# Performance work log

Measured on AMD Instinct MI355X. Metric: run time of the kernel, lower is better.

Reference implementation:

```python
import jax, jax.numpy as jnp
from jax import lax
import numpy as np

B, C_IN, C_OUT, H, W, K = 4, 128, 256, 64, 64, 3
KK = K * K
MID = C_IN // 4
EPS = 1e-5


def conv2d(x, w, b, pad, groups=1):
    out = lax.conv_general_dilated(x, w, (1, 1), [(pad, pad), (pad, pad)],
                                   feature_group_count=groups,
                                   dimension_numbers=('NCHW', 'OIHW', 'NCHW'))
    return out + b[None, :, None, None]


def bnorm(x, g, b, m, v):
    # inference-mode BatchNorm2d
    scale = (g / jnp.sqrt(v + EPS))
    return (x - m[None, :, None, None]) * scale[None, :, None, None] + b[None, :, None, None]


def bilinear_gather(x, py, px):
    # x: (B,C,H,W); py/px: (B,KK,H,W) float sample coords; zero outside bounds
    Bb, C, Hh, Ww = x.shape
    xf = x.reshape(Bb, C, Hh * Ww)
    y0 = jnp.floor(py)
    x0 = jnp.floor(px)
    wy1 = py - y0
    wx1 = px - x0

    def corner(yc, xc, wgt):
        valid = (yc >= 0) & (yc <= Hh - 1) & (xc >= 0) & (xc <= Ww - 1)
        yi = jnp.clip(yc, 0, Hh - 1).astype(jnp.int32)
        xi = jnp.clip(xc, 0, Ww - 1).astype(jnp.int32)
        idx = (yi * Ww + xi).reshape(Bb, -1)  # (B, KK*H*W)
        g = jax.vmap(lambda f, i: f[:, i])(xf, idx).reshape(Bb, C, *py.shape[1:])
        return g * (wgt * valid)[:, None]

    return (corner(y0, x0, (1 - wy1) * (1 - wx1))
            + corner(y0, x0 + 1, (1 - wy1) * wx1)
            + corner(y0 + 1, x0, wy1 * (1 - wx1))
            + corner(y0 + 1, x0 + 1, wy1 * wx1))


def deform_conv2d(x, offset, mask, w, b, pad=1):
    # modulated deformable conv v2, stride=1, dilation=1, groups=1, dg=1
    Bb, C, Hh, Ww = x.shape
    off = offset.reshape(Bb, KK, 2, Hh, Ww)  # (dy,dx) per kernel point
    k = jnp.arange(KK)
    ky = (k // K).astype(x.dtype)
    kx = (k % K).astype(x.dtype)
    py = (jnp.arange(Hh, dtype=x.dtype) - pad)[None, None, :, None] + ky[None, :, None, None] + off[:, :, 0]
    px = (jnp.arange(Ww, dtype=x.dtype) - pad)[None, None, None, :] + kx[None, :, None, None] + off[:, :, 1]
    val = bilinear_gather(x, py, px) * mask[:, None]  # (B,C,KK,H,W)
    return jnp.einsum('bckhw,ock->bohw', val, w.reshape(w.shape[0], C, KK)) + b[None, :, None, None]


def setup_inputs() -> dict:
    key = jax.random.key(0)
    ks = iter(jax.random.split(key, 40))

    def P(shape, scale=0.05):
        return jax.random.normal(next(ks), shape, jnp.float32) * scale

    d = {}
    d['x'] = jax.random.normal(next(ks), (B, C_IN, H, W), jnp.float32)
    # DCConv offset branch
    d['oc1_w'] = P((MID, C_IN, 3, 3)); d['oc1_b'] = P((MID,))
    d['obn_g'] = jnp.ones((MID,)); d['obn_b'] = jnp.zeros((MID,))
    d['obn_m'] = jnp.zeros((MID,)); d['obn_v'] = jnp.ones((MID,))
    d['oc2_w'] = P((2 * KK, MID, 3, 3), 0.01); d['oc2_b'] = P((2 * KK,), 0.01)
    # DCConv mask branch
    d['mc1_w'] = P((MID, C_IN, 3, 3)); d['mc1_b'] = P((MID,))
    d['mbn_g'] = jnp.ones((MID,)); d['mbn_b'] = jnp.zeros((MID,))
    d['mbn_m'] = jnp.zeros((MID,)); d['mbn_v'] = jnp.ones((MID,))
    d['mc2_w'] = P((KK, MID, 3, 3), 0.01); d['mc2_b'] = jnp.ones((KK,))
    # DCConv main weight
    d['dc_w'] = P((C_OUT, C_IN, 3, 3)); d['dc_b'] = jnp.zeros((C_OUT,))
    # contour branch: depthwise 3x3 + BN + ReLU + 1x1
    d['cb_dw_w'] = P((C_IN, 1, 3, 3)); d['cb_dw_b'] = P((C_IN,))
    d['cbn_g'] = jnp.ones((C_IN,)); d['cbn_b'] = jnp.zeros((C_IN,))
    d['cbn_m'] = jnp.zeros((C_IN,)); d['cbn_v'] = jnp.ones((C_IN,))
    d['cb_pw_w'] = P((C_OUT // 2, C_IN, 1, 1)); d['cb_pw_b'] = P((C_OUT // 2,))
    # spatial attention 7x7 -> 1 channel
    d['sa_w'] = P((1, C_OUT + C_OUT // 2, 7, 7)); d['sa_b'] = jnp.zeros((1,))
    # fusion 1x1 + BN + ReLU
    d['fu_w'] = P((C_OUT, C_OUT + C_OUT // 2, 1, 1)); d['fu_b'] = jnp.zeros((C_OUT,))
    d['fbn_g'] = jnp.ones((C_OUT,)); d['fbn_b'] = jnp.zeros((C_OUT,))
    d['fbn_m'] = jnp.zeros((C_OUT,)); d['fbn_v'] = jnp.ones((C_OUT,))
    return d


def reference(x, oc1_w, oc1_b, obn_g, obn_b, obn_m, obn_v, oc2_w, oc2_b,
              mc1_w, mc1_b, mbn_g, mbn_b, mbn_m, mbn_v, mc2_w, mc2_b,
              dc_w, dc_b, cb_dw_w, cb_dw_b, cbn_g, cbn_b, cbn_m, cbn_v,
              cb_pw_w, cb_pw_b, sa_w, sa_b, fu_w, fu_b, fbn_g, fbn_b, fbn_m, fbn_v):
    # DCConv: offsets + sigmoid masks + modulated deformable conv
    h = jax.nn.relu(bnorm(conv2d(x, oc1_w, oc1_b, 1), obn_g, obn_b, obn_m, obn_v))
    offset = conv2d(h, oc2_w, oc2_b, 1)
    hm = jax.nn.relu(bnorm(conv2d(x, mc1_w, mc1_b, 1), mbn_g, mbn_b, mbn_m, mbn_v))
    mask = jax.nn.sigmoid(conv2d(hm, mc2_w, mc2_b, 1))
    main_feat = deform_conv2d(x, offset, mask, dc_w, dc_b, pad=1)
    # contour branch
    hc = jax.nn.relu(bnorm(conv2d(x, cb_dw_w, cb_dw_b, 1, groups=C_IN), cbn_g, cbn_b, cbn_m, cbn_v))
    contour_feat = conv2d(hc, cb_pw_w, cb_pw_b, 0)
    combined = jnp.concatenate([main_feat, contour_feat], axis=1)
    attn = jax.nn.sigmoid(conv2d(combined, sa_w, sa_b, 3))
    combined = combined * attn
    return jax.nn.relu(bnorm(conv2d(combined, fu_w, fu_b, 0), fbn_g, fbn_b, fbn_m, fbn_v))
```

## Files before the change

kernel.cpp:

```cpp
#include <hip/hip_runtime.h>
#include <hip/hip_bf16.h>
#include <math.h>

#define BN   4
#define CIN  128
#define COUT 256
#define HWP  4096

typedef __hip_bfloat16 bf16;
typedef __attribute__((ext_vector_type(8))) short sh8;
typedef __attribute__((ext_vector_type(4))) float f32x4;

__device__ __forceinline__ float b2f(bf16 v) { return __bfloat162float(v); }
__device__ __forceinline__ float bflo(unsigned u) { return __uint_as_float(u << 16); }
__device__ __forceinline__ float bfhi(unsigned u) { return __uint_as_float(u & 0xffff0000u); }
__device__ __forceinline__ unsigned short f2bfbits(float f) {
    union { bf16 h; unsigned short u; } cv; cv.h = __float2bfloat16(f); return cv.u;
}
__device__ __forceinline__ float bfj(const uint4& c, int j) {
    unsigned u = (&c.x)[j >> 1];
    return (j & 1) ? bfhi(u) : bflo(u);
}

__global__ __launch_bounds__(256) void transpose_x_kernel(const float* __restrict__ x,
                                                          bf16* __restrict__ xt)
{
    __shared__ bf16 t[64][136];
    const int b = blockIdx.x >> 6, chunk = blockIdx.x & 63;
    const int pos0 = chunk * 64;
    const int tid = threadIdx.x;
    const int lane = tid & 63, wv = tid >> 6;
    const float* xb = x + (size_t)b * CIN * HWP + pos0 + lane;
    #pragma unroll 4
    for (int j = 0; j < 32; j++) {
        int ci = wv * 32 + j;
        t[lane][ci] = __float2bfloat16(xb[(size_t)ci * HWP]);
    }
    __syncthreads();
    const int p = tid >> 2, cig = tid & 3;
    uint4* dst = (uint4*)(xt + ((size_t)b * HWP + pos0 + p) * 128 + cig * 32);
    const uint4* src = (const uint4*)&t[p][cig * 32];
    #pragma unroll
    for (int q = 0; q < 4; q++) dst[q] = src[q];
}

__global__ __launch_bounds__(256) void prep_all_kernel(
    const float* __restrict__ dc_w,
    const float* __restrict__ oc1_w, const float* __restrict__ oc1_b,
    const float* __restrict__ obn_g, const float* __restrict__ obn_b,
    const float* __restrict__ obn_m, const float* __restrict__ obn_v,
    const float* __restrict__ mc1_w, const float* __restrict__ mc1_b,
    const float* __restrict__ mbn_g, const float* __restrict__ mbn_b,
    const float* __restrict__ mbn_m, const float* __restrict__ mbn_v,
    const float* __restrict__ fu_w, const float* __restrict__ fu_b,
    const float* __restrict__ fbn_g, const float* __restrict__ fbn_b,
    const float* __restrict__ fbn_m, const float* __restrict__ fbn_v,
    const float* __restrict__ sa_w,
    const float* __restrict__ oc2_w, const float* __restrict__ mc2_w,
    const float* __restrict__ cb_pw_w,
    const float* __restrict__ cb_dw_b, const float* __restrict__ cbn_g,
    const float* __restrict__ cbn_b, const float* __restrict__ cbn_m,
    const float* __restrict__ cbn_v,
    bf16* __restrict__ wBf2, bf16* __restrict__ wCf, float* __restrict__ ab,
    bf16* __restrict__ wFf, bf16* __restrict__ wSAf, float* __restrict__ fab,
    bf16* __restrict__ wDf, bf16* __restrict__ wPf, float* __restrict__ dwab)
{
    int o = blockIdx.x * 256 + threadIdx.x;
    if (o < 294912) {
        int j = o & 7, o2 = o >> 3;
        int lane = o2 & 63, t = o2 >> 6;
        int l16 = lane & 15, quad = lane >> 4;
        int mt = t & 3, t2 = t >> 2;
        int kt = t2 % 18, t3 = t2 / 18;
        int h = t3 & 1, wv = t3 >> 1;
        int co = wv * 64 + mt * 16 + l16;
        int kkh = kt * 32 + quad * 8 + j;
        int k = kkh >> 6, ci = h * 64 + (kkh & 63);
        wBf2[o] = __float2bfloat16(dc_w[co * 1152 + ci * 9 + k]);
    } else if (o < 368640) {
        int idx = o - 294912;
        int j = idx & 7, o2 = idx >> 3;
        int lane = o2 & 63, t = o2 >> 6;
        int l16 = lane & 15, quad = lane >> 4;
        int kt = t % 36, wv = t / 36;
        int co = wv * 16 + l16;
        int kk = kt * 32 + quad * 8 + j;
        int k = kk >> 7, ci = kk & 127;
        float v = (co < 32) ? oc1_w[co * 1152 + ci * 9 + k]
                            : mc1_w[(co - 32) * 1152 + ci * 9 + k];
        wCf[idx] = __float2bfloat16(v);
    } else if (o < 368704) {
        int c = o - 368640;
        float g, bb, m, vv, bias;
        if (c < 32) { g = obn_g[c]; bb = obn_b[c]; m = obn_m[c]; vv = obn_v[c]; bias = oc1_b[c]; }
        else { int c2 = c - 32; g = mbn_g[c2]; bb = mbn_b[c2]; m = mbn_m[c2]; vv = mbn_v[c2]; bias = mc1_b[c2]; }
        float alpha = g / sqrtf(vv + 1e-5f);
        ab[c] = alpha;
        ab[64 + c] = (bias - m) * alpha + bb;
    } else if (o < 467008) {
        int idx = o - 368704;
        int j = idx & 7, o2 = idx >> 3;
        int lane = o2 & 63, t = o2 >> 6;
        int l16 = lane & 15, quad = lane >> 4;
        int mt = t & 3, t2 = t >> 2;
        int kt = t2 % 12, wv = t2 / 12;
        int co = wv * 64 + mt * 16 + l16;
        int kk = kt * 32 + quad * 8 + j;
        wFf[idx] = __float2bfloat16(fu_w[co * 384 + kk]);
    } else if (o < 491584) {
        int idx = o - 467008;
        int j = idx & 7, o2 = idx >> 3;
        int lane = o2 & 63, t = o2 >> 6;
        int l16 = lane & 15, quad = lane >> 4;
        int kt = t % 12, wv = t / 12;
        int jr = wv * 16 + l16;
        int kk = kt * 32 + quad * 8 + j;
        wSAf[idx] = (jr < 49) ? __float2bfloat16(sa_w[kk * 49 + jr]) : __float2bfloat16(0.f);
    } else if (o < 491840) {
        int co = o - 491584;
        float alpha = fbn_g[co] / sqrtf(fbn_v[co] + 1e-5f);
        fab[co] = alpha;
        fab[256 + co] = (fu_b[co] - fbn_m[co]) * alpha + fbn_b[co];
    } else if (o < 510272) {
        int idx = o - 491840;
        int j = idx & 7, o2 = idx >> 3;
        int lane = o2 & 63, t = o2 >> 6;
        int l16 = lane & 15, quad = lane >> 4;
        int mt = t & 1, kt = t >> 1;
        int co = mt * 16 + l16;
        int kk = kt * 32 + quad * 8 + j;
        int k = kk >> 6, c = kk & 63;
        float v = 0.f;
        if (co < 18 && c < 32) v = oc2_w[co * 288 + c * 9 + k];
        else if (co >= 18 && co < 27 && c >= 32) v = mc2_w[(co - 18) * 288 + (c - 32) * 9 + k];
        wDf[idx] = __float2bfloat16(v);
    } else if (o < 526656) {
        int idx = o - 510272;
        int j = idx & 7, o2 = idx >> 3;
        int lane = o2 & 63, t = o2 >> 6;
        int l16 = lane & 15, quad = lane >> 4;
        int wv = t >> 3, kt = (t >> 1) & 3, mt = t & 1;
        int co = wv * 32 + mt * 16 + l16;
        int kk = kt * 32 + quad * 8 + j;
        wPf[idx] = __float2bfloat16(cb_pw_w[co * 128 + kk]);
    } else if (o < 526784) {
        int c = o - 526656;
        float alpha = cbn_g[c] / sqrtf(cbn_v[c] + 1e-5f);
        dwab[c] = alpha;
        dwab[128 + c] = (cb_dw_b[c] - cbn_m[c]) * alpha + cbn_b[c];
    }
}

__global__ __launch_bounds__(256) void conv1_mfma_kernel(
    const bf16* __restrict__ xt, const bf16* __restrict__ wCf, const float* __restrict__ ab,
    bf16* __restrict__ ht)
{
    __shared__ __align__(16) bf16 val[16][1160];

    const int bid = blockIdx.x;
    const int b = (bid & 7) >> 1;
    const int tile = ((bid >> 3) << 1) | (bid & 1);
    const int pos0 = tile * 16;
    const int y = tile >> 2, x0 = (tile & 3) * 16;
    const int tid = threadIdx.x;
    const int cig = tid & 15, pix = tid >> 4;
    const int ci0 = cig * 8;
    const int xxp = x0 + pix;

    const bf16* xtb = xt + (size_t)b * HWP * 128;
    #pragma unroll
    for (int k = 0; k < 9; k++) {
        int yy = y + k / 3 - 1, xx = xxp + k % 3 - 1;
        bool valid = (yy >= 0 && yy <= 63 && xx >= 0 && xx <= 63);
        uint4 c = {0, 0, 0, 0};
        if (valid) c = *(const uint4*)(xtb + (size_t)(yy * 64 + xx) * 128 + ci0);
        *(uint4*)&val[pix][k * 128 + ci0] = c;
    }
    __syncthreads();

    const int lane = tid & 63, wv = tid >> 6;
    const int quad = lane >> 4, l16 = lane & 15;
    f32x4 acc = {0, 0, 0, 0};
    const bf16* wl0 = wCf + (size_t)wv * 36 * 512 + lane * 8;
    const bf16* vbase = &val[l16][quad * 8];

    sh8 af = *(const sh8*)(wl0);
    sh8 bf = *(const sh8*)(vbase);
    sh8 afn, bfn;
    for (int kt = 0; kt < 36; kt++) {
        if (kt < 35) {
            afn = *(const sh8*)(wl0 + (kt + 1) * 512);
            bfn = *(const sh8*)(vbase + (kt + 1) * 32);
        }
        acc = __builtin_amdgcn_mfma_f32_16x16x32_bf16(af, bf, acc, 0, 0, 0);
        af = afn; bf = bfn;
    }

    float o0 = fmaxf(acc[0] * ab[wv * 16 + quad * 4 + 0] + ab[64 + wv * 16 + quad * 4 + 0], 0.f);
    float o1 = fmaxf(acc[1] * ab[wv * 16 + quad * 4 + 1] + ab[64 + wv * 16 + quad * 4 + 1], 0.f);
    float o2 = fmaxf(acc[2] * ab[wv * 16 + quad * 4 + 2] + ab[64 + wv * 16 + quad * 4 + 2], 0.f);
    float o3 = fmaxf(acc[3] * ab[wv * 16 + quad * 4 + 3] + ab[64 + wv * 16 + quad * 4 + 3], 0.f);
    uint2 pk;
    pk.x = (unsigned)f2bfbits(o0) | ((unsigned)f2bfbits(o1) << 16);
    pk.y = (unsigned)f2bfbits(o2) | ((unsigned)f2bfbits(o3) << 16);
    *(uint2*)(ht + ((size_t)b * HWP + pos0 + l16) * 64 + wv * 16 + quad * 4) = pk;
}

__global__ __launch_bounds__(256) void conv2_mfma_kernel(
    const bf16* __restrict__ ht, const bf16* __restrict__ wDf,
    const float* __restrict__ oc2_b, const float* __restrict__ mc2_b,
    float* __restrict__ offsb, float* __restrict__ mskb)
{
    __shared__ __align__(16) bf16 val[32][584];

    const int bid = blockIdx.x;
    const int b = bid >> 7, tile = bid & 127;
    const int y = tile >> 1, x0 = (tile & 1) * 32;
    const int tid = threadIdx.x;

    {
        const int cig = tid & 7, pix = tid >> 3;
        const int xxp = x0 + pix;
        const bf16* hb = ht + (size_t)b * HWP * 64;
        #pragma unroll
        for (int k = 0; k < 9; k++) {
            int yy = y + k / 3 - 1, xx = xxp + k % 3 - 1;
            bool valid = (yy >= 0 && yy <= 63 && xx >= 0 && xx <= 63);
            uint4 c = {0, 0, 0, 0};
            if (valid) c = *(const uint4*)(hb + (size_t)(yy * 64 + xx) * 64 + cig * 8);
            *(uint4*)&val[pix][k * 64 + cig * 8] = c;
        }
    }
    __syncthreads();

    const int lane = tid & 63, wv = tid >> 6;
    const int quad = lane >> 4, l16 = lane & 15;
    const int ph = wv >> 1, mt = wv & 1;
    f32x4 acc = {0, 0, 0, 0};
    const bf16* wl0 = wDf + ((size_t)mt * 64 + lane) * 8;
    const bf16* vbase = &val[ph * 16 + l16][quad * 8];

    sh8 af = *(const sh8*)(wl0);
    sh8 bf = *(const sh8*)(vbase);
    sh8 afn, bfn;
    for (int kt = 0; kt < 18; kt++) {
        if (kt < 17) {
            afn = *(const sh8*)(wl0 + (kt + 1) * 1024);
            bfn = *(const sh8*)(vbase + (kt + 1) * 32);
        }
        acc = __builtin_amdgcn_mfma_f32_16x16x32_bf16(af, bf, acc, 0, 0, 0);
        af = afn; bf = bfn;
    }

    const int pos = y * 64 + x0 + ph * 16 + l16;
    #pragma unroll
    for (int r = 0; r < 4; r++) {
        int co = mt * 16 + quad * 4 + r;
        if (co < 18) {
            offsb[(size_t)(b * 18 + co) * HWP + pos] = acc[r] + oc2_b[co];
        } else if (co < 27) {
            float s = acc[r] + mc2_b[co - 18];
            mskb[(size_t)(b * 9 + (co - 18)) * HWP + pos] = 1.f / (1.f + expf(-s));
        }
    }
}

__global__ __launch_bounds__(256) void dwpw_kernel(
    const bf16* __restrict__ xt, const float* __restrict__ dw_w, const float* __restrict__ dwab,
    const bf16* __restrict__ wPf, const float* __restrict__ pw_b, bf16* __restrict__ combined)
{
    __shared__ float wl[1152];
    __shared__ float abl[256];
    __shared__ __align__(16) bf16 vdw[16][136];
    const int bid = blockIdx.x;
    const int b = bid >> 8, tile = bid & 255;
    const int pos0 = tile * 16;
    const int y = tile >> 2, x0 = (tile & 3) * 16;
    const int tid = threadIdx.x;
    for (int i = tid; i < 1152; i += 256) wl[i] = dw_w[i];
    abl[tid] = dwab[tid];
    __syncthreads();

    {
        const int cig = tid & 15, pix = tid >> 4;
        const int ci0 = cig * 8;
        const int xxp = x0 + pix;
        const bf16* xtb = xt + (size_t)b * HWP * 128;
        float g[8] = {0, 0, 0, 0, 0, 0, 0, 0};
        #pragma unroll
        for (int k = 0; k < 9; k++) {
            int yy = y + k / 3 - 1, xx = xxp + k % 3 - 1;
            if (yy < 0 || yy > 63 || xx < 0 || xx > 63) continue;
            uint4 c = *(const uint4*)(xtb + (size_t)(yy * 64 + xx) * 128 + ci0);
            #pragma unroll
            for (int j = 0; j < 8; j++)
                g[j] += wl[(ci0 + j) * 9 + k] * bfj(c, j);
        }
        uint4 pk;
        float o[8];
        #pragma unroll
        for (int j = 0; j < 8; j++)
            o[j] = fmaxf(g[j] * abl[ci0 + j] + abl[128 + ci0 + j], 0.f);
        pk.x = (unsigned)f2bfbits(o[0]) | ((unsigned)f2bfbits(o[1]) << 16);
        pk.y = (unsigned)f2bfbits(o[2]) | ((unsigned)f2bfbits(o[3]) << 16);
        pk.z = (unsigned)f2bfbits(o[4]) | ((unsigned)f2bfbits(o[5]) << 16);
        pk.w = (unsigned)f2bfbits(o[6]) | ((unsigned)f2bfbits(o[7]) << 16);
        *(uint4*)&vdw[pix][ci0] = pk;
    }
    __syncthreads();

    const int lane = tid & 63, wv = tid >> 6;
    const int quad = lane >> 4, l16 = lane & 15;
    f32x4 acc[2] = {f32x4{0,0,0,0}, f32x4{0,0,0,0}};
    const bf16* fb = &vdw[l16][quad * 8];
    const bf16* wl0 = wPf + (size_t)wv * 4096 + lane * 8;
    #pragma unroll
    for (int kt = 0; kt < 4; kt++) {
        sh8 bf = *(const sh8*)(fb + kt * 32);
        #pragma unroll
        for (int mt = 0; mt < 2; mt++) {
            sh8 af = *(const sh8*)(wl0 + (kt * 2 + mt) * 512);
            acc[mt] = __builtin_amdgcn_mfma_f32_16x16x32_bf16(af, bf, acc[mt], 0, 0, 0);
        }
    }

    bf16* ct = combined + ((size_t)b * HWP + pos0 + l16) * 384 + 256;
    #pragma unroll
    for (int mt = 0; mt < 2; mt++) {
        int co_b = wv * 32 + mt * 16 + quad * 4;
        uint2 pk;
        pk.x = (unsigned)f2bfbits(acc[mt][0] + pw_b[co_b])     | ((unsigned)f2bfbits(acc[mt][1] + pw_b[co_b + 1]) << 16);
        pk.y = (unsigned)f2bfbits(acc[mt][2] + pw_b[co_b + 2]) | ((unsigned)f2bfbits(acc[mt][3] + pw_b[co_b + 3]) << 16);
        *(uint2*)(ct + co_b) = pk;
    }
}

__global__ __launch_bounds__(256) void deform_kernel(
    const bf16* __restrict__ xt, const float* __restrict__ offs, const float* __restrict__ msk,
    const bf16* __restrict__ wBf2, const float* __restrict__ bias, bf16* __restrict__ combined)
{
    __shared__ __align__(16) bf16 val[32][584];
    __shared__ int   ti[288][4];
    __shared__ float tw[288][4];

    const int bid = blockIdx.x;
    const int b = (bid & 7) >> 1;
    const int tile = ((bid >> 3) << 1) | (bid & 1);
    const int pos0 = tile * 32;
    const int tid = threadIdx.x;

    for (int e = tid; e < 288; e += 256) {
        int k = e >> 5, pix = e & 31;
        int pos = pos0 + pix;
        int y = pos >> 6, xc = pos & 63;
        float offy = offs[(size_t)(b * 18 + 2 * k) * HWP + pos];
        float offx = offs[(size_t)(b * 18 + 2 * k + 1) * HWP + pos];
        float m = msk[(size_t)(b * 9 + k) * HWP + pos];
        float py = (float)(y - 1 + k / 3) + offy;
        float px = (float)(xc - 1 + k % 3) + offx;
        float fy = floorf(py), fx = floorf(px);
        float wy1 = py - fy, wx1 = px - fx;
        int y0 = (int)fy, x0 = (int)fx;
        int y1 = y0 + 1, x1 = x0 + 1;
        bool vy0 = (y0 >= 0 && y0 <= 63), vy1 = (y1 >= 0 && y1 <= 63);
        bool vx0 = (x0 >= 0 && x0 <= 63), vx1 = (x1 >= 0 && x1 <= 63);
        int cy0 = min(max(y0, 0), 63), cy1 = min(max(y1, 0), 63);
        int cx0 = min(max(x0, 0), 63), cx1 = min(max(x1, 0), 63);
        ti[e][0] = cy0 * 64 + cx0;  tw[e][0] = (vy0 && vx0) ? (1.f - wy1) * (1.f - wx1) * m : 0.f;
        ti[e][1] = cy0 * 64 + cx1;  tw[e][1] = (vy0 && vx1) ? (1.f - wy1) * wx1 * m : 0.f;
        ti[e][2] = cy1 * 64 + cx0;  tw[e][2] = (vy1 && vx0) ? wy1 * (1.f - wx1) * m : 0.f;
        ti[e][3] = cy1 * 64 + cx1;  tw[e][3] = (vy1 && vx1) ? wy1 * wx1 * m : 0.f;
    }
    __syncthreads();

    const int lane = tid & 63, wv = tid >> 6;
    const int quad = lane >> 4, l16 = lane & 15;
    f32x4 acc[4][2] = {{f32x4{0,0,0,0}, f32x4{0,0,0,0}}, {f32x4{0,0,0,0}, f32x4{0,0,0,0}},
                       {f32x4{0,0,0,0}, f32x4{0,0,0,0}}, {f32x4{0,0,0,0}, f32x4{0,0,0,0}}};
    const bf16* xtb = xt + (size_t)b * HWP * 128;

    #pragma unroll
    for (int h = 0; h < 2; h++) {
        if (h) __syncthreads();
        {
            const int cig = tid & 7, pix = tid >> 3;
            const int ci0 = h * 64 + cig * 8;
            for (int k = 0; k < 9; k++) {
                const int e = k * 32 + pix;
                const int i0 = ti[e][0], i1 = ti[e][1], i2 = ti[e][2], i3 = ti[e][3];
                const float w0 = tw[e][0], w1 = tw[e][1], w2 = tw[e][2], w3 = tw[e][3];
                uint4 c0 = *(const uint4*)(xtb + (size_t)i0 * 128 + ci0);
                uint4 c1 = *(const uint4*)(xtb + (size_t)i1 * 128 + ci0);
                uint4 c2 = *(const uint4*)(xtb + (size_t)i2 * 128 + ci0);
                uint4 c3 = *(const uint4*)(xtb + (size_t)i3 * 128 + ci0);
                float g[8];
                #pragma unroll
                for (int j = 0; j < 8; j++)
                    g[j] = w0 * bfj(c0, j) + w1 * bfj(c1, j) + w2 * bfj(c2, j) + w3 * bfj(c3, j);
                uint4 pk;
                pk.x = (unsigned)f2bfbits(g[0]) | ((unsigned)f2bfbits(g[1]) << 16);
                pk.y = (unsigned)f2bfbits(g[2]) | ((unsigned)f2bfbits(g[3]) << 16);
                pk.z = (unsigned)f2bfbits(g[4]) | ((unsigned)f2bfbits(g[5]) << 16);
                pk.w = (unsigned)f2bfbits(g[6]) | ((unsigned)f2bfbits(g[7]) << 16);
                *(uint4*)&val[pix][k * 64 + cig * 8] = pk;
            }
        }
        __syncthreads();

        const bf16* wl0 = wBf2 + ((size_t)(wv * 2 + h) * 72) * 512 + lane * 8;
        const bf16* vb0 = &val[l16][quad * 8];
        const bf16* vb1 = &val[16 + l16][quad * 8];
        sh8 af[4], afn[4];
        #pragma unroll
        for (int mt = 0; mt < 4; mt++) af[mt] = *(const sh8*)(wl0 + mt * 512);
        for (int kt = 0; kt < 18; kt++) {
            sh8 b0 = *(const sh8*)(vb0 + kt * 32);
            sh8 b1 = *(const sh8*)(vb1 + kt * 32);
            if (kt < 17) {
                #pragma unroll
                for (int mt = 0; mt < 4; mt++)
                    afn[mt] = *(const sh8*)(wl0 + ((kt + 1) * 4 + mt) * 512);
            }
            #pragma unroll
            for (int mt = 0; mt < 4; mt++) {
                acc[mt][0] = __builtin_amdgcn_mfma_f32_16x16x32_bf16(af[mt], b0, acc[mt][0], 0, 0, 0);
                acc[mt][1] = __builtin_amdgcn_mfma_f32_16x16x32_bf16(af[mt], b1, acc[mt][1], 0, 0, 0);
            }
            #pragma unroll
            for (int mt = 0; mt < 4; mt++) af[mt] = afn[mt];
        }
    }

    #pragma unroll
    for (int ph = 0; ph < 2; ph++) {
        bf16* ct = combined + ((size_t)b * HWP + pos0 + ph * 16 + l16) * 384;
        #pragma unroll
        for (int mt = 0; mt < 4; mt++) {
            int co_b = wv * 64 + mt * 16 + quad * 4;
            uint2 pk;
            pk.x = (unsigned)f2bfbits(acc[mt][ph][0] + bias[co_b])     | ((unsigned)f2bfbits(acc[mt][ph][1] + bias[co_b + 1]) << 16);
            pk.y = (unsigned)f2bfbits(acc[mt][ph][2] + bias[co_b + 2]) | ((unsigned)f2bfbits(acc[mt][ph][3] + bias[co_b + 3]) << 16);
            *(uint2*)(ct + co_b) = pk;
        }
    }
}

__global__ __launch_bounds__(256) void sa_gemm_kernel(
    const bf16* __restrict__ combined, const bf16* __restrict__ wSAf, float* __restrict__ part)
{
    const int bid = blockIdx.x;
    const int b = bid >> 8, tile = bid & 255;
    const int pos0 = tile * 16;
    const int tid = threadIdx.x;
    const int lane = tid & 63, wv = tid >> 6;
    const int quad = lane >> 4, l16 = lane & 15;

    f32x4 acc = {0, 0, 0, 0};
    const bf16* fb = combined + ((size_t)b * HWP + pos0 + l16) * 384 + quad * 8;
    const bf16* wl0 = wSAf + (size_t)wv * 6144 + lane * 8;

    sh8 af = *(const sh8*)(wl0);
    sh8 bf = *(const sh8*)(fb);
    sh8 afn, bfn;
    for (int kt = 0; kt < 12; kt++) {
        if (kt < 11) {
            afn = *(const sh8*)(wl0 + (kt + 1) * 512);
            bfn = *(const sh8*)(fb + (kt + 1) * 32);
        }
        acc = __builtin_amdgcn_mfma_f32_16x16x32_bf16(af, bf, acc, 0, 0, 0);
        af = afn; bf = bfn;
    }
    #pragma unroll
    for (int r = 0; r < 4; r++) {
        int j = wv * 16 + quad * 4 + r;
        if (j < 49) part[(size_t)(j * BN + b) * HWP + pos0 + l16] = acc[r];
    }
}

__global__ __launch_bounds__(256) void fuse_kernel(
    const bf16* __restrict__ combined, const float* __restrict__ part, const float* __restrict__ sa_b,
    const bf16* __restrict__ wFf, const float* __restrict__ fab, float* __restrict__ out)
{
    __shared__ float sattn[16][17];
    __shared__ float lattn[16];

    const int bid = blockIdx.x;
    const int b = bid >> 8, tile = bid & 255;
    const int pos0 = tile * 16;
    const int y = tile >> 2, x0 = (tile & 3) * 16;
    const int tid = threadIdx.x;

    {
        const int px = tid & 15, g = tid >> 4;
        const int xp = x0 + px;
        float s = 0.f;
        for (int j = g; j < 49; j += 16) {
            int yy = y + j / 7 - 3, xx = xp + j % 7 - 3;
            if (yy < 0 || yy > 63 || xx < 0 || xx > 63) continue;
            s += part[(size_t)(j * BN + b) * HWP + yy * 64 + xx];
        }
        sattn[px][g] = s;
    }
    __syncthreads();
    if (tid < 16) {
        float t = sa_b[0];
        #pragma unroll
        for (int g = 0; g < 16; g++) t += sattn[tid][g];
        lattn[tid] = 1.f / (1.f + expf(-t));
    }
    __syncthreads();

    const int lane = tid & 63, wv = tid >> 6;
    const int quad = lane >> 4, l16 = lane & 15;

    f32x4 acc[4] = {f32x4{0,0,0,0}, f32x4{0,0,0,0}, f32x4{0,0,0,0}, f32x4{0,0,0,0}};
    const bf16* fb = combined + ((size_t)b * HWP + pos0 + l16) * 384 + quad * 8;
    const bf16* wl0 = wFf + (size_t)wv * 24576 + lane * 8;

    sh8 af[4], afn[4], bf, bfn;
    bf = *(const sh8*)(fb);
    #pragma unroll
    for (int mt = 0; mt < 4; mt++) af[mt] = *(const sh8*)(wl0 + mt * 512);
    for (int kt = 0; kt < 12; kt++) {
        if (kt < 11) {
            bfn = *(const sh8*)(fb + (kt + 1) * 32);
            #pragma unroll
            for (int mt = 0; mt < 4; mt++)
                afn[mt] = *(const sh8*)(wl0 + ((kt + 1) * 4 + mt) * 512);
        }
        #pragma unroll
        for (int mt = 0; mt < 4; mt++)
            acc[mt] = __builtin_amdgcn_mfma_f32_16x16x32_bf16(af[mt], bf, acc[mt], 0, 0, 0);
        bf = bfn;
        #pragma unroll
        for (int mt = 0; mt < 4; mt++) af[mt] = afn[mt];
    }

    float a = lattn[l16];
    float* op = out + (size_t)b * COUT * HWP + pos0 + l16;
    #pragma unroll
    for (int mt = 0; mt < 4; mt++) {
        int co_b = wv * 64 + mt * 16 + quad * 4;
        #pragma unroll
        for (int r = 0; r < 4; r++) {
            int co = co_b + r;
            float o = fmaxf(acc[mt][r] * a * fab[co] + fab[256 + co], 0.f);
            op[(size_t)co * HWP] = o;
        }
    }
}

extern "C" void kernel_launch(void* const* d_in, const int* in_sizes, int n_in,
                              void* d_out, int out_size, void* d_ws, size_t ws_size,
                              hipStream_t stream)
{
    const float* x      = (const float*)d_in[0];
    const float* oc1_w  = (const float*)d_in[1];
    const float* oc1_b  = (const float*)d_in[2];
    const float* obn_g  = (const float*)d_in[3];
    const float* obn_b  = (const float*)d_in[4];
    const float* obn_m  = (const float*)d_in[5];
    const float* obn_v  = (const float*)d_in[6];
    const float* oc2_w  = (const float*)d_in[7];
    const float* oc2_b  = (const float*)d_in[8];
    const float* mc1_w  = (const float*)d_in[9];
    const float* mc1_b  = (const float*)d_in[10];
    const float* mbn_g  = (const float*)d_in[11];
    const float* mbn_b  = (const float*)d_in[12];
    const float* mbn_m  = (const float*)d_in[13];
    const float* mbn_v  = (const float*)d_in[14];
    const float* mc2_w  = (const float*)d_in[15];
    const float* mc2_b  = (const float*)d_in[16];
    const float* dc_w   = (const float*)d_in[17];
    const float* dc_b   = (const float*)d_in[18];
    const float* cb_dw_w= (const float*)d_in[19];
    const float* cb_dw_b= (const float*)d_in[20];
    const float* cbn_g  = (const float*)d_in[21];
    const float* cbn_b  = (const float*)d_in[22];
    const float* cbn_m  = (const float*)d_in[23];
    const float* cbn_v  = (const float*)d_in[24];
    const float* cb_pw_w= (const float*)d_in[25];
    const float* cb_pw_b= (const float*)d_in[26];
    const float* sa_w   = (const float*)d_in[27];
    const float* sa_b   = (const float*)d_in[28];
    const float* fu_w   = (const float*)d_in[29];
    const float* fu_b   = (const float*)d_in[30];
    const float* fbn_g  = (const float*)d_in[31];
    const float* fbn_b  = (const float*)d_in[32];
    const float* fbn_m  = (const float*)d_in[33];
    const float* fbn_v  = (const float*)d_in[34];

    bf16*  ht    = (bf16*)d_ws;
    float* offsb = (float*)(ht + 1048576);
    float* mskb  = offsb + 294912;
    bf16*  comb  = (bf16*)(mskb + 147456);
    float* part  = (float*)(comb + 6291456);
    bf16*  xt    = (bf16*)(part + 802816);
    bf16*  wBf2  = xt + 2097152;
    bf16*  wCf   = wBf2 + 294912;
    float* ab    = (float*)(wCf + 73728);
    bf16*  wFf   = (bf16*)(ab + 128);
    bf16*  wSAf  = wFf + 98304;
    float* fab   = (float*)(wSAf + 24576);
    bf16*  wDf   = (bf16*)(fab + 512);
    bf16*  wPf   = wDf + 18432;
    float* dwab  = (float*)(wPf + 16384);

    float* out = (float*)d_out;

    transpose_x_kernel<<<256, 256, 0, stream>>>(x, xt);
    prep_all_kernel<<<2058, 256, 0, stream>>>(
        dc_w, oc1_w, oc1_b, obn_g, obn_b, obn_m, obn_v,
        mc1_w, mc1_b, mbn_g, mbn_b, mbn_m, mbn_v,
        fu_w, fu_b, fbn_g, fbn_b, fbn_m, fbn_v, sa_w,
        oc2_w, mc2_w, cb_pw_w, cb_dw_b, cbn_g, cbn_b, cbn_m, cbn_v,
        wBf2, wCf, ab, wFf, wSAf, fab, wDf, wPf, dwab);
    conv1_mfma_kernel<<<1024, 256, 0, stream>>>(xt, wCf, ab, ht);
    conv2_mfma_kernel<<<512, 256, 0, stream>>>(ht, wDf, oc2_b, mc2_b, offsb, mskb);
    dwpw_kernel<<<1024, 256, 0, stream>>>(xt, cb_dw_w, dwab, wPf, cb_pw_b, comb);
    deform_kernel<<<512, 256, 0, stream>>>(xt, offsb, mskb, wBf2, dc_b, comb);
    sa_gemm_kernel<<<1024, 256, 0, stream>>>(comb, wSAf, part);
    fuse_kernel<<<1024, 256, 0, stream>>>(comb, part, sa_b, wFf, fab, out);
}
```

Baseline: 212.9 us.

## Fuse offset/mask conv into deform kernel and transpose into prep kernel

Merges the x transpose into the weight-prep launch, retiles conv1 to 32-pixel tiles with a two-half channel split (reordered weight layout), and folds the second offset/mask convolution into the deformable conv kernel. The offsets and masks now stay in shared memory instead of passing through global buffers. This removes two launches and a global round trip. In exchange, the deform kernel carries extra prologue work and more shared memory, which may reduce occupancy.

New measurement: 207.0 us. -2.7%, faster.

```diff
diff --git a/kernel.cpp b/kernel.cpp
--- a/kernel.cpp
+++ b/kernel.cpp
@@ -22,29 +22,8 @@
     return (j & 1) ? bfhi(u) : bflo(u);
 }
 
-__global__ __launch_bounds__(256) void transpose_x_kernel(const float* __restrict__ x,
-                                                          bf16* __restrict__ xt)
-{
-    __shared__ bf16 t[64][136];
-    const int b = blockIdx.x >> 6, chunk = blockIdx.x & 63;
-    const int pos0 = chunk * 64;
-    const int tid = threadIdx.x;
-    const int lane = tid & 63, wv = tid >> 6;
-    const float* xb = x + (size_t)b * CIN * HWP + pos0 + lane;
-    #pragma unroll 4
-    for (int j = 0; j < 32; j++) {
-        int ci = wv * 32 + j;
-        t[lane][ci] = __float2bfloat16(xb[(size_t)ci * HWP]);
-    }
-    __syncthreads();
-    const int p = tid >> 2, cig = tid & 3;
-    uint4* dst = (uint4*)(xt + ((size_t)b * HWP + pos0 + p) * 128 + cig * 32);
-    const uint4* src = (const uint4*)&t[p][cig * 32];
-    #pragma unroll
-    for (int q = 0; q < 4; q++) dst[q] = src[q];
-}
-
 __global__ __launch_bounds__(256) void prep_all_kernel(
+    const float* __restrict__ x, bf16* __restrict__ xt,
     const float* __restrict__ dc_w,
     const float* __restrict__ oc1_w, const float* __restrict__ oc1_b,
     const float* __restrict__ obn_g, const float* __restrict__ obn_b,
@@ -61,16 +40,37 @@
     const float* __restrict__ cb_dw_b, const float* __restrict__ cbn_g,
     const float* __restrict__ cbn_b, const float* __restrict__ cbn_m,
     const float* __restrict__ cbn_v,
-    bf16* __restrict__ wBf2, bf16* __restrict__ wCf, float* __restrict__ ab,
+    bf16* __restrict__ wBf2, bf16* __restrict__ wCf2, float* __restrict__ ab,
     bf16* __restrict__ wFf, bf16* __restrict__ wSAf, float* __restrict__ fab,
     bf16* __restrict__ wDf, bf16* __restrict__ wPf, float* __restrict__ dwab)
 {
-    int o = blockIdx.x * 256 + threadIdx.x;
+    __shared__ bf16 t[64][136];
+    if (blockIdx.x < 256) {
+        const int b = blockIdx.x >> 6, chunk = blockIdx.x & 63;
+        const int pos0 = chunk * 64;
+        const int tid = threadIdx.x;
+        const int lane = tid & 63, wv = tid >> 6;
+        const float* xb = x + (size_t)b * CIN * HWP + pos0 + lane;
+        #pragma unroll 4
+        for (int j = 0; j < 32; j++) {
+            int ci = wv * 32 + j;
+            t[lane][ci] = __float2bfloat16(xb[(size_t)ci * HWP]);
+        }
+        __syncthreads();
+        const int p = tid >> 2, cig = tid & 3;
+        uint4* dst = (uint4*)(xt + ((size_t)b * HWP + pos0 + p) * 128 + cig * 32);
+        const uint4* src = (const uint4*)&t[p][cig * 32];
+        #pragma unroll
+        for (int q = 0; q < 4; q++) dst[q] = src[q];
+        return;
+    }
+
+    int o = (blockIdx.x - 256) * 256 + threadIdx.x;
     if (o < 294912) {
         int j = o & 7, o2 = o >> 3;
-        int lane = o2 & 63, t = o2 >> 6;
+        int lane = o2 & 63, t_ = o2 >> 6;
         int l16 = lane & 15, quad = lane >> 4;
-        int mt = t & 3, t2 = t >> 2;
+        int mt = t_ & 3, t2 = t_ >> 2;
         int kt = t2 % 18, t3 = t2 / 18;
         int h = t3 & 1, wv = t3 >> 1;
         int co = wv * 64 + mt * 16 + l16;
@@ -80,15 +80,16 @@
     } else if (o < 368640) {
         int idx = o - 294912;
         int j = idx & 7, o2 = idx >> 3;
-        int lane = o2 & 63, t = o2 >> 6;
+        int lane = o2 & 63, t_ = o2 >> 6;
         int l16 = lane & 15, quad = lane >> 4;
-        int kt = t % 36, wv = t / 36;
+        int kt = t_ % 18, t2 = t_ / 18;
+        int h = t2 & 1, wv = t2 >> 1;
         int co = wv * 16 + l16;
-        int kk = kt * 32 + quad * 8 + j;
-        int k = kk >> 7, ci = kk & 127;
+        int kkh = kt * 32 + quad * 8 + j;
+        int k = kkh >> 6, ci = h * 64 + (kkh & 63);
         float v = (co < 32) ? oc1_w[co * 1152 + ci * 9 + k]
                             : mc1_w[(co - 32) * 1152 + ci * 9 + k];
-        wCf[idx] = __float2bfloat16(v);
+        wCf2[idx] = __float2bfloat16(v);
     } else if (o < 368704) {
         int c = o - 368640;
         float g, bb, m, vv, bias;
@@ -100,9 +101,9 @@
     } else if (o < 467008) {
         int idx = o - 368704;
         int j = idx & 7, o2 = idx >> 3;
-        int lane = o2 & 63, t = o2 >> 6;
+        int lane = o2 & 63, t_ = o2 >> 6;
         int l16 = lane & 15, quad = lane >> 4;
-        int mt = t & 3, t2 = t >> 2;
+        int mt = t_ & 3, t2 = t_ >> 2;
         int kt = t2 % 12, wv = t2 / 12;
         int co = wv * 64 + mt * 16 + l16;
         int kk = kt * 32 + quad * 8 + j;
@@ -110,9 +111,9 @@
     } else if (o < 491584) {
         int idx = o - 467008;
         int j = idx & 7, o2 = idx >> 3;
-        int lane = o2 & 63, t = o2 >> 6;
+        int lane = o2 & 63, t_ = o2 >> 6;
         int l16 = lane & 15, quad = lane >> 4;
-        int kt = t % 12, wv = t / 12;
+        int kt = t_ % 12, wv = t_ / 12;
         int jr = wv * 16 + l16;
         int kk = kt * 32 + quad * 8 + j;
         wSAf[idx] = (jr < 49) ? __float2bfloat16(sa_w[kk * 49 + jr]) : __float2bfloat16(0.f);
@@ -124,9 +125,9 @@
     } else if (o < 510272) {
         int idx = o - 491840;
         int j = idx & 7, o2 = idx >> 3;
-        int lane = o2 & 63, t = o2 >> 6;
+        int lane = o2 & 63, t_ = o2 >> 6;
         int l16 = lane & 15, quad = lane >> 4;
-        int mt = t & 1, kt = t >> 1;
+        int mt = t_ & 1, kt = t_ >> 1;
         int co = mt * 16 + l16;
         int kk = kt * 32 + quad * 8 + j;
         int k = kk >> 6, c = kk & 63;
@@ -137,9 +138,9 @@
     } else if (o < 526656) {
         int idx = o - 510272;
         int j = idx & 7, o2 = idx >> 3;
-        int lane = o2 & 63, t = o2 >> 6;
+        int lane = o2 & 63, t_ = o2 >> 6;
         int l16 = lane & 15, quad = lane >> 4;
-        int wv = t >> 3, kt = (t >> 1) & 3, mt = t & 1;
+        int wv = t_ >> 3, kt = (t_ >> 1) & 3, mt = t_ & 1;
         int co = wv * 32 + mt * 16 + l16;
         int kk = kt * 32 + quad * 8 + j;
         wPf[idx] = __float2bfloat16(cb_pw_w[co * 128 + kk]);
@@ -152,116 +153,64 @@
 }
 
 __global__ __launch_bounds__(256) void conv1_mfma_kernel(
-    const bf16* __restrict__ xt, const bf16* __restrict__ wCf, const float* __restrict__ ab,
+    const bf16* __restrict__ xt, const bf16* __restrict__ wCf2, const float* __restrict__ ab,
     bf16* __restrict__ ht)
 {
-    __shared__ __align__(16) bf16 val[16][1160];
+    __shared__ __align__(16) bf16 val[32][584];
 
     const int bid = blockIdx.x;
     const int b = (bid & 7) >> 1;
     const int tile = ((bid >> 3) << 1) | (bid & 1);
-    const int pos0 = tile * 16;
-    const int y = tile >> 2, x0 = (tile & 3) * 16;
+    const int pos0 = tile * 32;
+    const int y = tile >> 1, x0 = (tile & 1) * 32;
     const int tid = threadIdx.x;
-    const int cig = tid & 15, pix = tid >> 4;
-    const int ci0 = cig * 8;
-    const int xxp = x0 + pix;
-
-    const bf16* xtb = xt + (size_t)b * HWP * 128;
-    #pragma unroll
-    for (int k = 0; k < 9; k++) {
-        int yy = y + k / 3 - 1, xx = xxp + k % 3 - 1;
-        bool valid = (yy >= 0 && yy <= 63 && xx >= 0 && xx <= 63);
-        uint4 c = {0, 0, 0, 0};
-        if (valid) c = *(const uint4*)(xtb + (size_t)(yy * 64 + xx) * 128 + ci0);
-        *(uint4*)&val[pix][k * 128 + ci0] = c;
-    }
-    __syncthreads();
-
     const int lane = tid & 63, wv = tid >> 6;
     const int quad = lane >> 4, l16 = lane & 15;
-    f32x4 acc = {0, 0, 0, 0};
-    const bf16* wl0 = wCf + (size_t)wv * 36 * 512 + lane * 8;
-    const bf16* vbase = &val[l16][quad * 8];
-
-    sh8 af = *(const sh8*)(wl0);
-    sh8 bf = *(const sh8*)(vbase);
-    sh8 afn, bfn;
-    for (int kt = 0; kt < 36; kt++) {
-        if (kt < 35) {
-            afn = *(const sh8*)(wl0 + (kt + 1) * 512);
-            bfn = *(const sh8*)(vbase + (kt + 1) * 32);
-        }
-        acc = __builtin_amdgcn_mfma_f32_16x16x32_bf16(af, bf, acc, 0, 0, 0);
-        af = afn; bf = bfn;
-    }
-
-    float o0 = fmaxf(acc[0] * ab[wv * 16 + quad * 4 + 0] + ab[64 + wv * 16 + quad * 4 + 0], 0.f);
-    float o1 = fmaxf(acc[1] * ab[wv * 16 + quad * 4 + 1] + ab[64 + wv * 16 + quad * 4 + 1], 0.f);
-    float o2 = fmaxf(acc[2] * ab[wv * 16 + quad * 4 + 2] + ab[64 + wv * 16 + quad * 4 + 2], 0.f);
-    float o3 = fmaxf(acc[3] * ab[wv * 16 + quad * 4 + 3] + ab[64 + wv * 16 + quad * 4 + 3], 0.f);
-    uint2 pk;
-    pk.x = (unsigned)f2bfbits(o0) | ((unsigned)f2bfbits(o1) << 16);
-    pk.y = (unsigned)f2bfbits(o2) | ((unsigned)f2bfbits(o3) << 16);
-    *(uint2*)(ht + ((size_t)b * HWP + pos0 + l16) * 64 + wv * 16 + quad * 4) = pk;
-}
-
-__global__ __launch_bounds__(256) void conv2_mfma_kernel(
-    const bf16* __restrict__ ht, const bf16* __restrict__ wDf,
-    const float* __restrict__ oc2_b, const float* __restrict__ mc2_b,
-    float* __restrict__ offsb, float* __restrict__ mskb)
-{
-    __shared__ __align__(16) bf16 val[32][584];
-
-    const int bid = blockIdx.x;
-    const int b = bid >> 7, tile = bid & 127;
-    const int y = tile >> 1, x0 = (tile & 1) * 32;
-    const int tid = threadIdx.x;
-
-    {
-        const int cig = tid & 7, pix = tid >> 3;
-        const int xxp = x0 + pix;
-        const bf16* hb = ht + (size_t)b * HWP * 64;
-        #pragma unroll
-        for (int k = 0; k < 9; k++) {
-            int yy = y + k / 3 - 1, xx = xxp + k % 3 - 1;
-            bool valid = (yy >= 0 && yy <= 63 && xx >= 0 && xx <= 63);
-            uint4 c = {0, 0, 0, 0};
-            if (valid) c = *(const uint4*)(hb + (size_t)(yy * 64 + xx) * 64 + cig * 8);
-            *(uint4*)&val[pix][k * 64 + cig * 8] = c;
-        }
-    }
-    __syncthreads();
-
-    const int lane = tid & 63, wv = tid >> 6;
-    const int quad = lane >> 4, l16 = lane & 15;
-    const int ph = wv >> 1, mt = wv & 1;
-    f32x4 acc = {0, 0, 0, 0};
-    const bf16* wl0 = wDf + ((size_t)mt * 64 + lane) * 8;
-    const bf16* vbase = &val[ph * 16 + l16][quad * 8];
-
-    sh8 af = *(const sh8*)(wl0);
-    sh8 bf = *(const sh8*)(vbase);
-    sh8 afn, bfn;
-    for (int kt = 0; kt < 18; kt++) {
-        if (kt < 17) {
-            afn = *(const sh8*)(wl0 + (kt + 1) * 1024);
-            bfn = *(const sh8*)(vbase + (kt + 1) * 32);
-        }
-        acc = __builtin_amdgcn_mfma_f32_16x16x32_bf16(af, bf, acc, 0, 0, 0);
-        af = afn; bf = bfn;
-    }
-
-    const int pos = y * 64 + x0 + ph * 16 + l16;
-    #pragma unroll
-    for (int r = 0; r < 4; r++) {
-        int co = mt * 16 + quad * 4 + r;
-        if (co < 18) {
-            offsb[(size_t)(b * 18 + co) * HWP + pos] = acc[r] + oc2_b[co];
-        } else if (co < 27) {
-            float s = acc[r] + mc2_b[co - 18];
-            mskb[(size_t)(b * 9 + (co - 18)) * HWP + pos] = 1.f / (1.f + expf(-s));
-        }
+
+    f32x4 acc[2] = {f32x4{0,0,0,0}, f32x4{0,0,0,0}};
+    const bf16* xtb = xt + (size_t)b * HWP * 128;
+
+    #pragma unroll
+    for (int h = 0; h < 2; h++) {
+        if (h) __syncthreads();
+        {
+            const int cig = tid & 7, pix = tid >> 3;
+            const int ci0 = h * 64 + cig * 8;
+            const int xxp = x0 + pix;
+            #pragma unroll
+            for (int k = 0; k < 9; k++) {
+                int yy = y + k / 3 - 1, xx = xxp + k % 3 - 1;
+                bool valid = (yy >= 0 && yy <= 63 && xx >= 0 && xx <= 63);
+                uint4 c = {0, 0, 0, 0};
+                if (valid) c = *(const uint4*)(xtb + (size_t)(yy * 64 + xx) * 128 + ci0);
+                *(uint4*)&val[pix][k * 64 + cig * 8] = c;
+            }
+        }
+        __syncthreads();
+
+        const bf16* wl0 = wCf2 + ((size_t)(wv * 2 + h) * 18) * 512 + lane * 8;
+        const bf16* vb0 = &val[l16][quad * 8];
+        const bf16* vb1 = &val[16 + l16][quad * 8];
+        for (int kt = 0; kt < 18; kt++) {
+            sh8 af = *(const sh8*)(wl0 + kt * 512);
+            sh8 b0 = *(const sh8*)(vb0 + kt * 32);
+            sh8 b1 = *(const sh8*)(vb1 + kt * 32);
+            acc[0] = __builtin_amdgcn_mfma_f32_16x16x32_bf16(af, b0, acc[0], 0, 0, 0);
+            acc[1] = __builtin_amdgcn_mfma_f32_16x16x32_bf16(af, b1, acc[1], 0, 0, 0);
+        }
+    }
+
+    const int co0 = wv * 16 + quad * 4;
+    #pragma unroll
+    for (int ph = 0; ph < 2; ph++) {
+        float o0 = fmaxf(acc[ph][0] * ab[co0 + 0] + ab[64 + co0 + 0], 0.f);
+        float o1 = fmaxf(acc[ph][1] * ab[co0 + 1] + ab[64 + co0 + 1], 0.f);
+        float o2 = fmaxf(acc[ph][2] * ab[co0 + 2] + ab[64 + co0 + 2], 0.f);
+        float o3 = fmaxf(acc[ph][3] * ab[co0 + 3] + ab[64 + co0 + 3], 0.f);
+        uint2 pk;
+        pk.x = (unsigned)f2bfbits(o0) | ((unsigned)f2bfbits(o1) << 16);
+        pk.y = (unsigned)f2bfbits(o2) | ((unsigned)f2bfbits(o3) << 16);
+        *(uint2*)(ht + ((size_t)b * HWP + pos0 + ph * 16 + l16) * 64 + co0) = pk;
     }
 }
 
@@ -336,36 +285,80 @@
 }
 
 __global__ __launch_bounds__(256) void deform_kernel(
-    const bf16* __restrict__ xt, const float* __restrict__ offs, const float* __restrict__ msk,
+    const bf16* __restrict__ xt, const bf16* __restrict__ ht, const bf16* __restrict__ wDf,
+    const float* __restrict__ oc2_b, const float* __restrict__ mc2_b,
     const bf16* __restrict__ wBf2, const float* __restrict__ bias, bf16* __restrict__ combined)
 {
     __shared__ __align__(16) bf16 val[32][584];
     __shared__ int   ti[288][4];
     __shared__ float tw[288][4];
+    __shared__ float loff[18][32];
+    __shared__ float lmsk[9][32];
 
     const int bid = blockIdx.x;
     const int b = (bid & 7) >> 1;
     const int tile = ((bid >> 3) << 1) | (bid & 1);
     const int pos0 = tile * 32;
+    const int y = tile >> 1, x0 = (tile & 1) * 32;
     const int tid = threadIdx.x;
+    const int lane = tid & 63, wv = tid >> 6;
+    const int quad = lane >> 4, l16 = lane & 15;
+
+    {
+        const int cig = tid & 7, pix = tid >> 3;
+        const int xxp = x0 + pix;
+        const bf16* hb = ht + (size_t)b * HWP * 64;
+        #pragma unroll
+        for (int k = 0; k < 9; k++) {
+            int yy = y + k / 3 - 1, xx = xxp + k % 3 - 1;
+            bool valid = (yy >= 0 && yy <= 63 && xx >= 0 && xx <= 63);
+            uint4 c = {0, 0, 0, 0};
+            if (valid) c = *(const uint4*)(hb + (size_t)(yy * 64 + xx) * 64 + cig * 8);
+            *(uint4*)&val[pix][k * 64 + cig * 8] = c;
+        }
+    }
+    __syncthreads();
+    {
+        const int ph = wv >> 1, mt = wv & 1;
+        f32x4 acc2 = {0, 0, 0, 0};
+        const bf16* wl0 = wDf + ((size_t)mt * 64 + lane) * 8;
+        const bf16* vbase = &val[ph * 16 + l16][quad * 8];
+        for (int kt = 0; kt < 18; kt++) {
+            sh8 af = *(const sh8*)(wl0 + kt * 1024);
+            sh8 bf = *(const sh8*)(vbase + kt * 32);
+            acc2 = __builtin_amdgcn_mfma_f32_16x16x32_bf16(af, bf, acc2, 0, 0, 0);
+        }
+        const int pix2 = ph * 16 + l16;
+        #pragma unroll
+        for (int r = 0; r < 4; r++) {
+            int co = mt * 16 + quad * 4 + r;
+            if (co < 18) {
+                loff[co][pix2] = acc2[r] + oc2_b[co];
+            } else if (co < 27) {
+                float s = acc2[r] + mc2_b[co - 18];
+                lmsk[co - 18][pix2] = 1.f / (1.f + expf(-s));
+            }
+        }
+    }
+    __syncthreads();
 
     for (int e = tid; e < 288; e += 256) {
         int k = e >> 5, pix = e & 31;
         int pos = pos0 + pix;
-        int y = pos >> 6, xc = pos & 63;
-        float offy = offs[(size_t)(b * 18 + 2 * k) * HWP + pos];
-        float offx = offs[(size_t)(b * 18 + 2 * k + 1) * HWP + pos];
-        float m = msk[(size_t)(b * 9 + k) * HWP + pos];
-        float py = (float)(y - 1 + k / 3) + offy;
+        int yp = pos >> 6, xc = pos & 63;
+        float offy = loff[2 * k][pix];
+        float offx = loff[2 * k + 1][pix];
+        float m = lmsk[k][pix];
+        float py = (float)(yp - 1 + k / 3) + offy;
         float px = (float)(xc - 1 + k % 3) + offx;
         float fy = floorf(py), fx = floorf(px);
         float wy1 = py - fy, wx1 = px - fx;
-        int y0 = (int)fy, x0 = (int)fx;
-        int y1 = y0 + 1, x1 = x0 + 1;
+        int y0 = (int)fy, x0c = (int)fx;
+        int y1 = y0 + 1, x1 = x0c + 1;
         bool vy0 = (y0 >= 0 && y0 <= 63), vy1 = (y1 >= 0 && y1 <= 63);
-        bool vx0 = (x0 >= 0 && x0 <= 63), vx1 = (x1 >= 0 && x1 <= 63);
+        bool vx0 = (x0c >= 0 && x0c <= 63), vx1 = (x1 >= 0 && x1 <= 63);
         int cy0 = min(max(y0, 0), 63), cy1 = min(max(y1, 0), 63);
-        int cx0 = min(max(x0, 0), 63), cx1 = min(max(x1, 0), 63);
+        int cx0 = min(max(x0c, 0), 63), cx1 = min(max(x1, 0), 63);
         ti[e][0] = cy0 * 64 + cx0;  tw[e][0] = (vy0 && vx0) ? (1.f - wy1) * (1.f - wx1) * m : 0.f;
         ti[e][1] = cy0 * 64 + cx1;  tw[e][1] = (vy0 && vx1) ? (1.f - wy1) * wx1 * m : 0.f;
         ti[e][2] = cy1 * 64 + cx0;  tw[e][2] = (vy1 && vx0) ? wy1 * (1.f - wx1) * m : 0.f;
@@ -373,8 +366,6 @@
     }
     __syncthreads();
 
-    const int lane = tid & 63, wv = tid >> 6;
-    const int quad = lane >> 4, l16 = lane & 15;
     f32x4 acc[4][2] = {{f32x4{0,0,0,0}, f32x4{0,0,0,0}}, {f32x4{0,0,0,0}, f32x4{0,0,0,0}},
                        {f32x4{0,0,0,0}, f32x4{0,0,0,0}}, {f32x4{0,0,0,0}, f32x4{0,0,0,0}}};
     const bf16* xtb = xt + (size_t)b * HWP * 128;
@@ -591,14 +582,12 @@
     const float* fbn_v  = (const float*)d_in[34];
 
     bf16*  ht    = (bf16*)d_ws;
-    float* offsb = (float*)(ht + 1048576);
-    float* mskb  = offsb + 294912;
-    bf16*  comb  = (bf16*)(mskb + 147456);
+    bf16*  comb  = ht + 1048576;
     float* part  = (float*)(comb + 6291456);
     bf16*  xt    = (bf16*)(part + 802816);
     bf16*  wBf2  = xt + 2097152;
-    bf16*  wCf   = wBf2 + 294912;
-    float* ab    = (float*)(wCf + 73728);
+    bf16*  wCf2  = wBf2 + 294912;
+    float* ab    = (float*)(wCf2 + 73728);
     bf16*  wFf   = (bf16*)(ab + 128);
     bf16*  wSAf  = wFf + 98304;
     float* fab   = (float*)(wSAf + 24576);
@@ -608,17 +597,16 @@
 
     float* out = (float*)d_out;
 
-    transpose_x_kernel<<<256, 256, 0, stream>>>(x, xt);
-    prep_all_kernel<<<2058, 256, 0, stream>>>(
+    prep_all_kernel<<<256 + 2058, 256, 0, stream>>>(
+        x, xt,
         dc_w, oc1_w, oc1_b, obn_g, obn_b, obn_m, obn_v,
         mc1_w, mc1_b, mbn_g, mbn_b, mbn_m, mbn_v,
         fu_w, fu_b, fbn_g, fbn_b, fbn_m, fbn_v, sa_w,
         oc2_w, mc2_w, cb_pw_w, cb_dw_b, cbn_g, cbn_b, cbn_m, cbn_v,
-        wBf2, wCf, ab, wFf, wSAf, fab, wDf, wPf, dwab);
-    conv1_mfma_kernel<<<1024, 256, 0, stream>>>(xt, wCf, ab, ht);
-    conv2_mfma_kernel<<<512, 256, 0, stream>>>(ht, wDf, oc2_b, mc2_b, offsb, mskb);
+        wBf2, wCf2, ab, wFf, wSAf, fab, wDf, wPf, dwab);
+    conv1_mfma_kernel<<<512, 256, 0, stream>>>(xt, wCf2, ab, ht);
     dwpw_kernel<<<1024, 256, 0, stream>>>(xt, cb_dw_w, dwab, wPf, cb_pw_b, comb);
-    deform_kernel<<<512, 256, 0, stream>>>(xt, offsb, mskb, wBf2, dc_b, comb);
+    deform_kernel<<<512, 256, 0, stream>>>(xt, ht, wDf, oc2_b, mc2_b, wBf2, dc_b, comb);
     sa_gemm_kernel<<<1024, 256, 0, stream>>>(comb, wSAf, part);
     fuse_kernel<<<1024, 256, 0, stream>>>(comb, part, sa_b, wFf, fab, out);
 }
```
